# Kernel optimization log

Measured on AMD Instinct MI355X. Metric: run time of the kernel, lower is better.

## Reference

```python
import jax, jax.numpy as jnp
import numpy as np

SIZE = (2, 2)


def setup_inputs() -> dict:
    key = jax.random.key(0)
    k1, k2 = jax.random.split(key)
    B, H, W, C = 16, 64, 64, 128
    out_size = B * H * SIZE[0] * W * SIZE[1] * C  # 33_554_432
    updates = jax.random.normal(k1, (B, H, W, C), dtype=jnp.float32)
    mask = jax.random.randint(k2, (B, H, W, C), 0, out_size, dtype=jnp.int32)
    return {"updates": updates, "mask": mask}


def reference(updates, mask):
    # MaxUnpooling2D: scatter flattened updates into a zero buffer of the
    # full (upsampled) output size using flattened argmax indices, then reshape.
    B, H, W, C = updates.shape
    out_h, out_w = H * SIZE[0], W * SIZE[1]
    out_size = B * out_h * out_w * C
    # tf.scatter_nd sums duplicate indices -> use .add (matches semantics)
    flat = jnp.zeros((out_size,), dtype=updates.dtype).at[mask.reshape(-1)].add(
        updates.reshape(-1)
    )
    return flat.reshape(B, out_h, out_w, C)
```

## Files before the change

kernel.cpp:

```cpp
#include <hip/hip_runtime.h>


#define NB        2048
#define NB_SHIFT  14
#define RB        16384
#define P1B       1024
#define IPB       8192

__global__ __launch_bounds__(256) void partition_kernel(
        const float4* __restrict__ upd4,
        const int4*   __restrict__ mask4,
        unsigned int* __restrict__ table,
        uint2*        __restrict__ pairs) {
    __shared__ unsigned int hb[NB];
    __shared__ unsigned int tsum[256];
    __shared__ uint2 stage[IPB];
    const int t = threadIdx.x;
    const int k = blockIdx.x;
    const int s4 = k * (IPB / 4);

    for (int b = t; b < NB; b += 256) hb[b] = 0u;
    __syncthreads();

    int4 mm[IPB / 4 / 256];
    #pragma unroll
    for (int j = 0; j < IPB / 4 / 256; ++j) mm[j] = mask4[s4 + j * 256 + t];
    #pragma unroll
    for (int j = 0; j < IPB / 4 / 256; ++j) {
        atomicAdd(&hb[((unsigned)mm[j].x) >> NB_SHIFT], 1u);
        atomicAdd(&hb[((unsigned)mm[j].y) >> NB_SHIFT], 1u);
        atomicAdd(&hb[((unsigned)mm[j].z) >> NB_SHIFT], 1u);
        atomicAdd(&hb[((unsigned)mm[j].w) >> NB_SHIFT], 1u);
    }
    __syncthreads();

    unsigned c[8], s = 0;
    #pragma unroll
    for (int j = 0; j < 8; ++j) { c[j] = hb[t * 8 + j]; s += c[j]; }
    tsum[t] = s;
    __syncthreads();
    #pragma unroll
    for (int d = 1; d < 256; d <<= 1) {
        unsigned v = (t >= d) ? tsum[t - d] : 0u;
        __syncthreads();
        tsum[t] += v;
        __syncthreads();
    }
    unsigned run = (t > 0) ? tsum[t - 1] : 0u;
    #pragma unroll
    for (int j = 0; j < 8; ++j) {
        unsigned b = t * 8 + j;
        hb[b] = run;
        table[(size_t)k * NB + b] = run | (c[j] << 16);
        run += c[j];
    }
    __syncthreads();

    float4 uu[IPB / 4 / 256];
    #pragma unroll
    for (int j = 0; j < IPB / 4 / 256; ++j) uu[j] = upd4[s4 + j * 256 + t];
    #pragma unroll
    for (int j = 0; j < IPB / 4 / 256; ++j) {
        #define PLACE(mi, vi) { \
            unsigned b_ = ((unsigned)(mi)) >> NB_SHIFT; \
            unsigned pos_ = atomicAdd(&hb[b_], 1u); \
            stage[pos_] = make_uint2(((unsigned)(mi)) & (RB - 1u), __float_as_uint(vi)); }
        PLACE(mm[j].x, uu[j].x)
        PLACE(mm[j].y, uu[j].y)
        PLACE(mm[j].z, uu[j].z)
        PLACE(mm[j].w, uu[j].w)
        #undef PLACE
    }
    __syncthreads();

    const uint4* sp = (const uint4*)stage;
    uint4* dp = (uint4*)(pairs + (size_t)k * IPB);
    #pragma unroll
    for (int j = 0; j < IPB / 2 / 256; ++j) dp[j * 256 + t] = sp[j * 256 + t];
}

__global__ __launch_bounds__(256) void unbin_kernel(
        const unsigned int* __restrict__ table,
        const uint2*        __restrict__ pairs,
        float4*             __restrict__ out4) {
    extern __shared__ float tile[];
    const int b = blockIdx.x, t = threadIdx.x;
    float4* t4 = (float4*)tile;

    for (int j = t; j < RB / 4; j += 256) t4[j] = make_float4(0.f, 0.f, 0.f, 0.f);
    __syncthreads();

    unsigned e[P1B / 256];
    #pragma unroll
    for (int j = 0; j < P1B / 256; ++j)
        e[j] = table[(size_t)(t + j * 256) * NB + b];
    #pragma unroll
    for (int j = 0; j < P1B / 256; ++j) {
        unsigned start = e[j] & 0xFFFFu, cnt = e[j] >> 16;
        const uint2* p = pairs + (size_t)(t + j * 256) * IPB + start;
        for (unsigned i = 0; i < cnt; ++i) {
            uint2 pr = p[i];
            atomicAdd(&tile[pr.x], __uint_as_float(pr.y));
        }
    }
    __syncthreads();

    for (int j = t; j < RB / 4; j += 256)
        out4[(size_t)b * (RB / 4) + j] = t4[j];
}

__global__ void zero_out_kernel(float4* __restrict__ out, int n4) {
    int i = blockIdx.x * blockDim.x + threadIdx.x;
    if (i < n4) out[i] = make_float4(0.f, 0.f, 0.f, 0.f);
}
__global__ void scatter_add_kernel(const float4* __restrict__ upd,
                                   const int4* __restrict__ mask,
                                   float* __restrict__ out, int n4) {
    int i = blockIdx.x * blockDim.x + threadIdx.x;
    if (i < n4) {
        float4 u = upd[i];
        int4 m = mask[i];
        atomicAdd(out + m.x, u.x);
        atomicAdd(out + m.y, u.y);
        atomicAdd(out + m.z, u.z);
        atomicAdd(out + m.w, u.w);
    }
}

extern "C" void kernel_launch(void* const* d_in, const int* in_sizes, int n_in,
                              void* d_out, int out_size, void* d_ws, size_t ws_size,
                              hipStream_t stream) {
    const float* updates = (const float*)d_in[0];
    const int*   mask    = (const int*)d_in[1];
    float* out = (float*)d_out;
    const int n  = in_sizes[0];
    const int n4 = n >> 2;
    const int o4 = out_size >> 2;

    const size_t need = (size_t)P1B * IPB * sizeof(uint2)
                      + (size_t)P1B * NB * sizeof(unsigned);
    if (ws_size >= need && out_size == NB * RB && n == P1B * IPB) {
        uint2* pairs = (uint2*)d_ws;
        unsigned int* table = (unsigned int*)((char*)d_ws + (size_t)P1B * IPB * sizeof(uint2));

        partition_kernel<<<P1B, 256, 0, stream>>>(
            (const float4*)updates, (const int4*)mask, table, pairs);
        unbin_kernel<<<NB, 256, RB * sizeof(float), stream>>>(
            table, pairs, (float4*)out);
    } else {
        zero_out_kernel<<<(o4 + 255) / 256, 256, 0, stream>>>((float4*)out, o4);
        scatter_add_kernel<<<(n4 + 255) / 256, 256, 0, stream>>>(
            (const float4*)updates, (const int4*)mask, out, n4);
    }
}
```

Before: 268.8 us.

## Transpose bin table and load-balance unbin work via prefix-sum and binary search

Adds a tiled transpose kernel so that each unbin block reads its column of per-partition bin offsets contiguously instead of with a large stride. The unbin kernel now prefix-sums the per-chunk counts across the block with wave shuffles and gives each thread a flat element index, mapped back to its chunk by binary search in shared memory. This replaces the per-thread serial loops over variable-length chunks, which caused load imbalance and divergence. The cost is an extra kernel launch, an extra 8 MB table round trip, and a 10-step binary search per element.

Measured after the change: 298.4 us. 11.0% more time.

```diff
diff --git a/kernel.cpp b/kernel.cpp
--- a/kernel.cpp
+++ b/kernel.cpp
@@ -10,7 +10,7 @@
 __global__ __launch_bounds__(256) void partition_kernel(
         const float4* __restrict__ upd4,
         const int4*   __restrict__ mask4,
-        unsigned int* __restrict__ table,
+        unsigned int* __restrict__ tableA,
         uint2*        __restrict__ pairs) {
     __shared__ unsigned int hb[NB];
     __shared__ unsigned int tsum[256];
@@ -51,7 +51,7 @@
     for (int j = 0; j < 8; ++j) {
         unsigned b = t * 8 + j;
         hb[b] = run;
-        table[(size_t)k * NB + b] = run | (c[j] << 16);
+        tableA[(size_t)k * NB + b] = run | (c[j] << 16);
         run += c[j];
     }
     __syncthreads();
@@ -79,29 +79,70 @@
     for (int j = 0; j < IPB / 2 / 256; ++j) dp[j * 256 + t] = sp[j * 256 + t];
 }
 
+__global__ __launch_bounds__(256) void transpose_kernel(
+        const unsigned int* __restrict__ A, unsigned int* __restrict__ B) {
+    __shared__ unsigned int tile[32][33];
+    const int tx = threadIdx.x & 31, ty = threadIdx.x >> 5;
+    const int bx = blockIdx.x;
+    const int by = blockIdx.y;
+    #pragma unroll
+    for (int r = 0; r < 32; r += 8)
+        tile[ty + r][tx] = A[(size_t)(by * 32 + ty + r) * NB + bx * 32 + tx];
+    __syncthreads();
+    #pragma unroll
+    for (int r = 0; r < 32; r += 8)
+        B[(size_t)(bx * 32 + ty + r) * P1B + by * 32 + tx] = tile[tx][ty + r];
+}
+
 __global__ __launch_bounds__(256) void unbin_kernel(
-        const unsigned int* __restrict__ table,
+        const unsigned int* __restrict__ tableB,
         const uint2*        __restrict__ pairs,
         float4*             __restrict__ out4) {
     extern __shared__ float tile[];
+    __shared__ unsigned choff[P1B];
+    __shared__ unsigned chbase[P1B];
+    __shared__ unsigned wpart[4];
+    __shared__ unsigned Ttot;
     const int b = blockIdx.x, t = threadIdx.x;
     float4* t4 = (float4*)tile;
 
     for (int j = t; j < RB / 4; j += 256) t4[j] = make_float4(0.f, 0.f, 0.f, 0.f);
+
+    uint4 e = ((const uint4*)(tableB + (size_t)b * P1B))[t];
+    unsigned c0 = e.x >> 16, c1 = e.y >> 16, c2 = e.z >> 16, c3 = e.w >> 16;
+    unsigned s = c0 + c1 + c2 + c3;
+
+    unsigned inc = s;
+    #pragma unroll
+    for (int d = 1; d < 64; d <<= 1) {
+        unsigned v = __shfl_up(inc, d, 64);
+        if ((t & 63) >= d) inc += v;
+    }
+    if ((t & 63) == 63) wpart[t >> 6] = inc;
+    __syncthreads();
+    unsigned wbase = 0;
+    #pragma unroll
+    for (int w = 0; w < 4; ++w) if (w < (t >> 6)) wbase += wpart[w];
+    unsigned ex = wbase + inc - s;
+
+    const unsigned k0 = t * 4;
+    choff[k0 + 0] = ex;                 chbase[k0 + 0] = (k0 + 0) * IPB + (e.x & 0xFFFFu);
+    choff[k0 + 1] = ex + c0;            chbase[k0 + 1] = (k0 + 1) * IPB + (e.y & 0xFFFFu);
+    choff[k0 + 2] = ex + c0 + c1;       chbase[k0 + 2] = (k0 + 2) * IPB + (e.z & 0xFFFFu);
+    choff[k0 + 3] = ex + c0 + c1 + c2;  chbase[k0 + 3] = (k0 + 3) * IPB + (e.w & 0xFFFFu);
+    if (t == 255) Ttot = ex + s;
     __syncthreads();
 
-    unsigned e[P1B / 256];
-    #pragma unroll
-    for (int j = 0; j < P1B / 256; ++j)
-        e[j] = table[(size_t)(t + j * 256) * NB + b];
-    #pragma unroll
-    for (int j = 0; j < P1B / 256; ++j) {
-        unsigned start = e[j] & 0xFFFFu, cnt = e[j] >> 16;
-        const uint2* p = pairs + (size_t)(t + j * 256) * IPB + start;
-        for (unsigned i = 0; i < cnt; ++i) {
-            uint2 pr = p[i];
-            atomicAdd(&tile[pr.x], __uint_as_float(pr.y));
+    const unsigned T = Ttot;
+    for (unsigned i = t; i < T; i += 256) {
+        unsigned k = 0;
+        #pragma unroll
+        for (unsigned stp = 512; stp; stp >>= 1) {
+            unsigned nk = k + stp;
+            if (nk < P1B && choff[nk] <= i) k = nk;
         }
+        uint2 pr = pairs[chbase[k] + (i - choff[k])];
+        atomicAdd(&tile[pr.x], __uint_as_float(pr.y));
     }
     __syncthreads();
 
@@ -137,16 +178,19 @@
     const int n4 = n >> 2;
     const int o4 = out_size >> 2;
 
-    const size_t need = (size_t)P1B * IPB * sizeof(uint2)
-                      + (size_t)P1B * NB * sizeof(unsigned);
+    const size_t pairs_b  = (size_t)P1B * IPB * sizeof(uint2);
+    const size_t table_b  = (size_t)P1B * NB * sizeof(unsigned);
+    const size_t need = pairs_b + 2 * table_b;
     if (ws_size >= need && out_size == NB * RB && n == P1B * IPB) {
         uint2* pairs = (uint2*)d_ws;
-        unsigned int* table = (unsigned int*)((char*)d_ws + (size_t)P1B * IPB * sizeof(uint2));
+        unsigned* tableA = (unsigned*)((char*)d_ws + pairs_b);
+        unsigned* tableB = (unsigned*)((char*)d_ws + pairs_b + table_b);
 
         partition_kernel<<<P1B, 256, 0, stream>>>(
-            (const float4*)updates, (const int4*)mask, table, pairs);
+            (const float4*)updates, (const int4*)mask, tableA, pairs);
+        transpose_kernel<<<dim3(NB / 32, P1B / 32), 256, 0, stream>>>(tableA, tableB);
         unbin_kernel<<<NB, 256, RB * sizeof(float), stream>>>(
-            table, pairs, (float4*)out);
+            tableB, pairs, (float4*)out);
     } else {
         zero_out_kernel<<<(o4 + 255) / 256, 256, 0, stream>>>((float4*)out, o4);
         scatter_add_kernel<<<(n4 + 255) / 256, 256, 0, stream>>>(
```
